# Performance work log

Measured on AMD Instinct MI355X. Metric: run time of the kernel, lower is better.

Reference implementation:

```python
import jax, jax.numpy as jnp
import numpy as np

C1, C2 = 128, 128

def _glorot(key, shape):
    fan_in = shape[-1]
    return jax.random.normal(key, shape, dtype=jnp.float32) / np.sqrt(fan_in)

def setup_inputs() -> dict:
    key = jax.random.key(0)
    ks = jax.random.split(key, 12)
    b, n = 16, 64
    x = jax.random.normal(ks[0], (b, n, 16), dtype=jnp.float32)
    # 1x1 Conv1d weights stored as [out, in]
    e1_w = _glorot(ks[1], (128, 3));    e1_b = jnp.zeros((128,), jnp.float32)
    e2_w = _glorot(ks[2], (128, 13));   e2_b = jnp.zeros((128,), jnp.float32)
    r1_w = _glorot(ks[3], (256, 128));  r1_b = jnp.zeros((256,), jnp.float32)
    r2_w = _glorot(ks[4], (512, 256));  r2_b = jnp.zeros((512,), jnp.float32)
    r3_w = _glorot(ks[5], (1024, 512)); r3_b = jnp.zeros((1024,), jnp.float32)
    w1   = _glorot(ks[6], (512, 2048)); b1   = jnp.zeros((512,), jnp.float32)
    w2   = _glorot(ks[7], (2048, 512)); b2   = jnp.zeros((2048,), jnp.float32)
    return {"x": x, "e1_w": e1_w, "e1_b": e1_b, "e2_w": e2_w, "e2_b": e2_b,
            "r1_w": r1_w, "r1_b": r1_b, "r2_w": r2_w, "r2_b": r2_b,
            "r3_w": r3_w, "r3_b": r3_b, "w1": w1, "b1": b1, "w2": w2, "b2": b2}

def reference(x, e1_w, e1_b, e2_w, e2_b, r1_w, r1_b, r2_w, r2_b, r3_w, r3_b, w1, b1, w2, b2):
    # x: [b, n, 16]; coord = first 3 dims, pos = last 13 (one-hot-like keypoint id)
    coord, pos = x[:, :, :3], x[:, :, 3:]
    # 1x1 Conv1d == per-point linear. E1/E2 each have their own ReLU, then sum.
    emb = (jax.nn.relu(jnp.einsum('bnc,oc->bno', coord, e1_w) + e1_b)
           + jax.nn.relu(jnp.einsum('bnc,oc->bno', pos, e2_w) + e2_b))  # [b,n,128]
    # refine_E: three 1x1 conv + relu stages -> [b,n,1024]
    emb = jax.nn.relu(jnp.einsum('bnc,oc->bno', emb, r1_w) + r1_b)
    emb = jax.nn.relu(jnp.einsum('bnc,oc->bno', emb, r2_w) + r2_b)
    emb = jax.nn.relu(jnp.einsum('bnc,oc->bno', emb, r3_w) + r3_b)
    # Pairwise layer1: cat((emb_i, emb_j), ch) with emb_i[b,c,i,j]=emb[b,c,j],
    # emb_j[b,c,i,j]=emb[b,c,i]. A 1x1 conv on the concat decomposes into
    # two matmuls applied to emb, broadcast-added pairwise (never forming the
    # [b,2048,n,n] tensor).
    w1a, w1b = w1[:, :1024], w1[:, 1024:]
    A = jnp.einsum('bnc,oc->bno', emb, w1a)  # depends on j
    B = jnp.einsum('bnc,oc->bno', emb, w1b)  # depends on i
    h1 = jax.nn.relu(B[:, :, None, :] + A[:, None, :, :] + b1)  # [b,i,j,512]
    # reduction='mean' over (i,j); layer2 (1x1 conv, linear) commutes with mean
    m = jnp.mean(h1, axis=(1, 2))                 # [b,512]
    out = jnp.einsum('bc,oc->bo', m, w2) + b2     # [b,2048]
    return out
```

## Files before the change

### kernel.cpp

```cpp
#include <hip/hip_runtime.h>


typedef __attribute__((ext_vector_type(8))) short s16x8;
typedef __attribute__((ext_vector_type(8))) unsigned short u16x8;
typedef __attribute__((ext_vector_type(4))) float f32x4;

static __device__ __forceinline__ unsigned short f2bf(float f) {
    unsigned u = __float_as_uint(f);
    u += 0x7fff + ((u >> 16) & 1);
    return (unsigned short)(u >> 16);
}

__global__ __launch_bounds__(256) void k_embed(
    const float* __restrict__ x,
    const float* __restrict__ e1w, const float* __restrict__ e1b,
    const float* __restrict__ e2w, const float* __restrict__ e2b,
    unsigned short* __restrict__ emb0b)
{
    int idx = blockIdx.x * 256 + threadIdx.x;
    int row = idx >> 7, o = idx & 127;
    const float* xr = x + row * 16;
    float s1 = e1b[o] + xr[0] * e1w[o * 3 + 0] + xr[1] * e1w[o * 3 + 1] + xr[2] * e1w[o * 3 + 2];
    float s2 = e2b[o];
#pragma unroll
    for (int k = 0; k < 13; ++k) s2 += xr[3 + k] * e2w[o * 13 + k];
    emb0b[row * 128 + o] = f2bf(fmaxf(s1, 0.f) + fmaxf(s2, 0.f));
}

__global__ __launch_bounds__(256) void k_convw(
    const float* __restrict__ r1w, const float* __restrict__ r2w,
    const float* __restrict__ r3w, const float* __restrict__ w1,
    unsigned short* __restrict__ r1b, unsigned short* __restrict__ r2b,
    unsigned short* __restrict__ r3b, unsigned short* __restrict__ wab)
{
    const int n1 = 256 * 128, n2 = 512 * 256, n3 = 1024 * 512;
    int i = (blockIdx.x * 256 + threadIdx.x) * 4;
    float4 v; unsigned short* dst; int j;
    if (i < n1)                { j = i;             v = *(const float4*)(r1w + j); dst = r1b + j; }
    else if (i < n1 + n2)      { j = i - n1;        v = *(const float4*)(r2w + j); dst = r2b + j; }
    else if (i < n1 + n2 + n3) { j = i - n1 - n2;   v = *(const float4*)(r3w + j); dst = r3b + j; }
    else {
        j = i - n1 - n2 - n3;
        int n = j >> 10, k = j & 1023;
        v = *(const float4*)(w1 + (size_t)(n & 511) * 2048 + (n >> 9) * 1024 + k);
        dst = wab + j;
    }
    ushort4 o; o.x = f2bf(v.x); o.y = f2bf(v.y); o.z = f2bf(v.z); o.w = f2bf(v.w);
    *(ushort4*)dst = o;
}

__global__ __launch_bounds__(256) void k_mgemm(
    const unsigned short* __restrict__ A, const unsigned short* __restrict__ W,
    const float* __restrict__ bias, float* __restrict__ Cf,
    unsigned short* __restrict__ Cb, int K, int N, int relu)
{
    __shared__ unsigned short As[64 * 72];
    __shared__ unsigned short Ws[64 * 72];
    int t = threadIdx.x;
    int m0 = blockIdx.x * 64, n0 = blockIdx.y * 64;
    int lane = t & 63, wv = t >> 6;
    int wm = (wv >> 1) * 32, wn = (wv & 1) * 32;
    int lr = lane & 15, quad = lane >> 4;

    f32x4 acc[2][2] = {};

    int srow = t >> 3;
    int scol = (t & 7) * 8;

    for (int k0 = 0; k0 < K; k0 += 64) {
        u16x8 a0 = *(const u16x8*)(A + (size_t)(m0 + srow) * K + k0 + scol);
        u16x8 a1 = *(const u16x8*)(A + (size_t)(m0 + srow + 32) * K + k0 + scol);
        u16x8 w0 = *(const u16x8*)(W + (size_t)(n0 + srow) * K + k0 + scol);
        u16x8 w1 = *(const u16x8*)(W + (size_t)(n0 + srow + 32) * K + k0 + scol);
        __syncthreads();
        *(u16x8*)(As + srow * 72 + scol)        = a0;
        *(u16x8*)(As + (srow + 32) * 72 + scol) = a1;
        *(u16x8*)(Ws + srow * 72 + scol)        = w0;
        *(u16x8*)(Ws + (srow + 32) * 72 + scol) = w1;
        __syncthreads();
#pragma unroll
        for (int kk = 0; kk < 64; kk += 32) {
            s16x8 af[2], bfr[2];
#pragma unroll
            for (int mt = 0; mt < 2; ++mt)
                af[mt] = *(const s16x8*)(As + (wm + mt * 16 + lr) * 72 + kk + quad * 8);
#pragma unroll
            for (int nt = 0; nt < 2; ++nt)
                bfr[nt] = *(const s16x8*)(Ws + (wn + nt * 16 + lr) * 72 + kk + quad * 8);
#pragma unroll
            for (int mt = 0; mt < 2; ++mt)
#pragma unroll
                for (int nt = 0; nt < 2; ++nt)
                    acc[mt][nt] = __builtin_amdgcn_mfma_f32_16x16x32_bf16(
                        af[mt], bfr[nt], acc[mt][nt], 0, 0, 0);
        }
    }

#pragma unroll
    for (int mt = 0; mt < 2; ++mt)
#pragma unroll
        for (int nt = 0; nt < 2; ++nt) {
            int col = n0 + wn + nt * 16 + lr;
            float bv = bias ? bias[col] : 0.f;
#pragma unroll
            for (int r = 0; r < 4; ++r) {
                int row = m0 + wm + mt * 16 + quad * 4 + r;
                float v = acc[mt][nt][r] + bv;
                if (relu) v = fmaxf(v, 0.f);
                if (Cb) Cb[(size_t)row * N + col] = f2bf(v);
                else    Cf[(size_t)row * N + col] = v;
            }
        }
}

__global__ __launch_bounds__(256) void k_pairmean(
    const float* __restrict__ AB, const float* __restrict__ b1,
    float* __restrict__ msum)
{
    __shared__ float sA[64 * 64];
    __shared__ float sB[16 * 64];
    __shared__ float sb1[64];
    __shared__ float sPart[4][64];
    int t = threadIdx.x;
    int b = blockIdx.x, c0 = blockIdx.y * 64, z = blockIdx.z;
    int cl = t & 63, ig = t >> 6;

#pragma unroll
    for (int rep = 0; rep < 4; ++rep) {
        int lin = rep * 256 + t;
        int j = lin >> 4, cq = (lin & 15) * 4;
        float4 v = *(const float4*)(AB + (size_t)(b * 64 + j) * 1024 + c0 + cq);
        *(float4*)&sA[j * 64 + cq] = v;
    }
    {
        int i = t >> 4, cq = (t & 15) * 4;
        float4 v = *(const float4*)(AB + (size_t)(b * 64 + z * 16 + i) * 1024 + 512 + c0 + cq);
        *(float4*)&sB[i * 64 + cq] = v;
    }
    if (t < 64) sb1[t] = b1[c0 + t];
    __syncthreads();

    float av[64];
#pragma unroll
    for (int j = 0; j < 64; ++j) av[j] = sA[j * 64 + cl];
    float b1c = sb1[cl];
    float s = 0.f;
#pragma unroll
    for (int ii = 0; ii < 4; ++ii) {
        float base = sB[(ig * 4 + ii) * 64 + cl] + b1c;
#pragma unroll
        for (int j = 0; j < 64; ++j) s += fmaxf(base + av[j], 0.f);
    }
    sPart[ig][cl] = s;
    __syncthreads();
    if (t < 64) {
        float tot = sPart[0][t] + sPart[1][t] + sPart[2][t] + sPart[3][t];
        atomicAdd(&msum[b * 512 + c0 + t], tot);
    }
}

__global__ __launch_bounds__(256) void k_final(
    const float* __restrict__ msum, const float* __restrict__ w2,
    const float* __restrict__ b2, float* __restrict__ out)
{
    __shared__ float sm[512];
    int t = threadIdx.x;
    int b = blockIdx.x;
    int o = blockIdx.y * 256 + t;
    sm[t]       = msum[b * 512 + t]       * (1.f / 4096.f);
    sm[t + 256] = msum[b * 512 + 256 + t] * (1.f / 4096.f);
    __syncthreads();
    const float* wr = w2 + (size_t)o * 512;
    float acc = 0.f;
#pragma unroll 8
    for (int c = 0; c < 512; c += 4) {
        float4 w = *(const float4*)(wr + c);
        acc += sm[c] * w.x + sm[c + 1] * w.y + sm[c + 2] * w.z + sm[c + 3] * w.w;
    }
    out[b * 2048 + o] = acc + b2[o];
}

extern "C" void kernel_launch(void* const* d_in, const int* in_sizes, int n_in,
                              void* d_out, int out_size, void* d_ws, size_t ws_size,
                              hipStream_t stream)
{
    const float* x   = (const float*)d_in[0];
    const float* e1w = (const float*)d_in[1];
    const float* e1b = (const float*)d_in[2];
    const float* e2w = (const float*)d_in[3];
    const float* e2b = (const float*)d_in[4];
    const float* r1w = (const float*)d_in[5];
    const float* r1b = (const float*)d_in[6];
    const float* r2w = (const float*)d_in[7];
    const float* r2b = (const float*)d_in[8];
    const float* r3w = (const float*)d_in[9];
    const float* r3b = (const float*)d_in[10];
    const float* w1  = (const float*)d_in[11];
    const float* b1  = (const float*)d_in[12];
    const float* w2  = (const float*)d_in[13];
    const float* b2  = (const float*)d_in[14];
    float* out = (float*)d_out;

    unsigned short* emb0b = (unsigned short*)d_ws;
    unsigned short* emb1b = emb0b + 1024 * 128;
    unsigned short* emb2b = emb1b + 1024 * 256;
    unsigned short* emb3b = emb2b + 1024 * 512;
    unsigned short* r1wb  = emb3b + 1024 * 1024;
    unsigned short* r2wb  = r1wb  + 256 * 128;
    unsigned short* r3wb  = r2wb  + 512 * 256;
    unsigned short* wab   = r3wb  + 1024 * 512;
    float* AB   = (float*)(wab + 1024 * 1024);
    float* msum = AB + 1024 * 1024;

    hipMemsetAsync(msum, 0, 16 * 512 * sizeof(float), stream);

    k_convw<<<1696, 256, 0, stream>>>(r1w, r2w, r3w, w1, r1wb, r2wb, r3wb, wab);
    k_embed<<<512, 256, 0, stream>>>(x, e1w, e1b, e2w, e2b, emb0b);

    k_mgemm<<<dim3(16, 4),  256, 0, stream>>>(emb0b, r1wb, r1b, nullptr, emb1b, 128, 256, 1);
    k_mgemm<<<dim3(16, 8),  256, 0, stream>>>(emb1b, r2wb, r2b, nullptr, emb2b, 256, 512, 1);
    k_mgemm<<<dim3(16, 16), 256, 0, stream>>>(emb2b, r3wb, r3b, nullptr, emb3b, 512, 1024, 1);
    k_mgemm<<<dim3(16, 16), 256, 0, stream>>>(emb3b, wab, nullptr, AB, nullptr, 1024, 1024, 0);

    k_pairmean<<<dim3(16, 8, 4), 256, 0, stream>>>(AB, b1, msum);
    k_final<<<dim3(16, 8), 256, 0, stream>>>(msum, w2, b2, out);
}
```

Baseline: 140.6 us.

## Merge setup kernels with memset, halve GEMM M-tile, prefetch next K-slice

The weight-conversion kernel, the embedding kernel and the msum memset become one launch, split by block-index range. The GEMM M tile drops from 64 to 32 rows, doubling the grid for better CU occupancy on these small GEMMs. Global loads for the next K slice are register-prefetched to overlap with MFMA work. Each block now reuses the W tile across fewer rows, so total W traffic rises.

After: 132.7 us. -5.7%, faster.

```diff
diff --git a/kernel.cpp b/kernel.cpp
--- a/kernel.cpp
+++ b/kernel.cpp
@@ -11,42 +11,47 @@
     return (unsigned short)(u >> 16);
 }
 
-__global__ __launch_bounds__(256) void k_embed(
+__global__ __launch_bounds__(256) void k_setup(
     const float* __restrict__ x,
     const float* __restrict__ e1w, const float* __restrict__ e1b,
     const float* __restrict__ e2w, const float* __restrict__ e2b,
-    unsigned short* __restrict__ emb0b)
-{
-    int idx = blockIdx.x * 256 + threadIdx.x;
-    int row = idx >> 7, o = idx & 127;
-    const float* xr = x + row * 16;
-    float s1 = e1b[o] + xr[0] * e1w[o * 3 + 0] + xr[1] * e1w[o * 3 + 1] + xr[2] * e1w[o * 3 + 2];
-    float s2 = e2b[o];
-#pragma unroll
-    for (int k = 0; k < 13; ++k) s2 += xr[3 + k] * e2w[o * 13 + k];
-    emb0b[row * 128 + o] = f2bf(fmaxf(s1, 0.f) + fmaxf(s2, 0.f));
-}
-
-__global__ __launch_bounds__(256) void k_convw(
     const float* __restrict__ r1w, const float* __restrict__ r2w,
     const float* __restrict__ r3w, const float* __restrict__ w1,
-    unsigned short* __restrict__ r1b, unsigned short* __restrict__ r2b,
-    unsigned short* __restrict__ r3b, unsigned short* __restrict__ wab)
-{
-    const int n1 = 256 * 128, n2 = 512 * 256, n3 = 1024 * 512;
-    int i = (blockIdx.x * 256 + threadIdx.x) * 4;
-    float4 v; unsigned short* dst; int j;
-    if (i < n1)                { j = i;             v = *(const float4*)(r1w + j); dst = r1b + j; }
-    else if (i < n1 + n2)      { j = i - n1;        v = *(const float4*)(r2w + j); dst = r2b + j; }
-    else if (i < n1 + n2 + n3) { j = i - n1 - n2;   v = *(const float4*)(r3w + j); dst = r3b + j; }
-    else {
-        j = i - n1 - n2 - n3;
-        int n = j >> 10, k = j & 1023;
-        v = *(const float4*)(w1 + (size_t)(n & 511) * 2048 + (n >> 9) * 1024 + k);
-        dst = wab + j;
-    }
-    ushort4 o; o.x = f2bf(v.x); o.y = f2bf(v.y); o.z = f2bf(v.z); o.w = f2bf(v.w);
-    *(ushort4*)dst = o;
+    unsigned short* __restrict__ emb0b,
+    unsigned short* __restrict__ r1wb, unsigned short* __restrict__ r2wb,
+    unsigned short* __restrict__ r3wb, unsigned short* __restrict__ wab,
+    float* __restrict__ msum)
+{
+    int blk = blockIdx.x;
+    if (blk < 1696) {
+        const int n1 = 256 * 128, n2 = 512 * 256, n3 = 1024 * 512;
+        int i = (blk * 256 + threadIdx.x) * 4;
+        float4 v; unsigned short* dst; int j;
+        if (i < n1)                { j = i;           v = *(const float4*)(r1w + j); dst = r1wb + j; }
+        else if (i < n1 + n2)      { j = i - n1;      v = *(const float4*)(r2w + j); dst = r2wb + j; }
+        else if (i < n1 + n2 + n3) { j = i - n1 - n2; v = *(const float4*)(r3w + j); dst = r3wb + j; }
+        else {
+            j = i - n1 - n2 - n3;
+            int n = j >> 10, k = j & 1023;
+            v = *(const float4*)(w1 + (size_t)(n & 511) * 2048 + (n >> 9) * 1024 + k);
+            dst = wab + j;
+        }
+        ushort4 o; o.x = f2bf(v.x); o.y = f2bf(v.y); o.z = f2bf(v.z); o.w = f2bf(v.w);
+        *(ushort4*)dst = o;
+    } else if (blk < 2208) {
+        int idx = (blk - 1696) * 256 + threadIdx.x;
+        int row = idx >> 7, o = idx & 127;
+        const float* xr = x + row * 16;
+        float s1 = e1b[o] + xr[0] * e1w[o * 3 + 0] + xr[1] * e1w[o * 3 + 1] + xr[2] * e1w[o * 3 + 2];
+        float s2 = e2b[o];
+#pragma unroll
+        for (int k = 0; k < 13; ++k) s2 += xr[3 + k] * e2w[o * 13 + k];
+        emb0b[row * 128 + o] = f2bf(fmaxf(s1, 0.f) + fmaxf(s2, 0.f));
+    } else {
+        int i = ((blk - 2208) * 256 + threadIdx.x) * 4;
+        float4 z = {0.f, 0.f, 0.f, 0.f};
+        *(float4*)(msum + i) = z;
+    }
 }
 
 __global__ __launch_bounds__(256) void k_mgemm(
@@ -54,63 +59,60 @@
     const float* __restrict__ bias, float* __restrict__ Cf,
     unsigned short* __restrict__ Cb, int K, int N, int relu)
 {
-    __shared__ unsigned short As[64 * 72];
+    __shared__ unsigned short As[32 * 72];
     __shared__ unsigned short Ws[64 * 72];
     int t = threadIdx.x;
-    int m0 = blockIdx.x * 64, n0 = blockIdx.y * 64;
+    int m0 = blockIdx.x * 32, n0 = blockIdx.y * 64;
     int lane = t & 63, wv = t >> 6;
-    int wm = (wv >> 1) * 32, wn = (wv & 1) * 32;
+    int wm = (wv >> 1) * 16, wn = (wv & 1) * 32;
     int lr = lane & 15, quad = lane >> 4;
 
-    f32x4 acc[2][2] = {};
+    f32x4 acc[2] = {};
 
     int srow = t >> 3;
     int scol = (t & 7) * 8;
+    const unsigned short* Ap  = A + (size_t)(m0 + srow) * K + scol;
+    const unsigned short* Wp0 = W + (size_t)(n0 + srow) * K + scol;
+    const unsigned short* Wp1 = W + (size_t)(n0 + srow + 32) * K + scol;
+
+    u16x8 ra = *(const u16x8*)Ap;
+    u16x8 rw0 = *(const u16x8*)Wp0;
+    u16x8 rw1 = *(const u16x8*)Wp1;
 
     for (int k0 = 0; k0 < K; k0 += 64) {
-        u16x8 a0 = *(const u16x8*)(A + (size_t)(m0 + srow) * K + k0 + scol);
-        u16x8 a1 = *(const u16x8*)(A + (size_t)(m0 + srow + 32) * K + k0 + scol);
-        u16x8 w0 = *(const u16x8*)(W + (size_t)(n0 + srow) * K + k0 + scol);
-        u16x8 w1 = *(const u16x8*)(W + (size_t)(n0 + srow + 32) * K + k0 + scol);
         __syncthreads();
-        *(u16x8*)(As + srow * 72 + scol)        = a0;
-        *(u16x8*)(As + (srow + 32) * 72 + scol) = a1;
-        *(u16x8*)(Ws + srow * 72 + scol)        = w0;
-        *(u16x8*)(Ws + (srow + 32) * 72 + scol) = w1;
+        *(u16x8*)(As + srow * 72 + scol)        = ra;
+        *(u16x8*)(Ws + srow * 72 + scol)        = rw0;
+        *(u16x8*)(Ws + (srow + 32) * 72 + scol) = rw1;
         __syncthreads();
+        if (k0 + 64 < K) {
+            ra  = *(const u16x8*)(Ap  + k0 + 64);
+            rw0 = *(const u16x8*)(Wp0 + k0 + 64);
+            rw1 = *(const u16x8*)(Wp1 + k0 + 64);
+        }
 #pragma unroll
         for (int kk = 0; kk < 64; kk += 32) {
-            s16x8 af[2], bfr[2];
-#pragma unroll
-            for (int mt = 0; mt < 2; ++mt)
-                af[mt] = *(const s16x8*)(As + (wm + mt * 16 + lr) * 72 + kk + quad * 8);
-#pragma unroll
-            for (int nt = 0; nt < 2; ++nt)
-                bfr[nt] = *(const s16x8*)(Ws + (wn + nt * 16 + lr) * 72 + kk + quad * 8);
-#pragma unroll
-            for (int mt = 0; mt < 2; ++mt)
-#pragma unroll
-                for (int nt = 0; nt < 2; ++nt)
-                    acc[mt][nt] = __builtin_amdgcn_mfma_f32_16x16x32_bf16(
-                        af[mt], bfr[nt], acc[mt][nt], 0, 0, 0);
-        }
-    }
-
-#pragma unroll
-    for (int mt = 0; mt < 2; ++mt)
-#pragma unroll
-        for (int nt = 0; nt < 2; ++nt) {
-            int col = n0 + wn + nt * 16 + lr;
-            float bv = bias ? bias[col] : 0.f;
-#pragma unroll
-            for (int r = 0; r < 4; ++r) {
-                int row = m0 + wm + mt * 16 + quad * 4 + r;
-                float v = acc[mt][nt][r] + bv;
-                if (relu) v = fmaxf(v, 0.f);
-                if (Cb) Cb[(size_t)row * N + col] = f2bf(v);
-                else    Cf[(size_t)row * N + col] = v;
-            }
-        }
+            s16x8 af  = *(const s16x8*)(As + (wm + lr) * 72 + kk + quad * 8);
+            s16x8 bf0 = *(const s16x8*)(Ws + (wn + lr) * 72 + kk + quad * 8);
+            s16x8 bf1 = *(const s16x8*)(Ws + (wn + 16 + lr) * 72 + kk + quad * 8);
+            acc[0] = __builtin_amdgcn_mfma_f32_16x16x32_bf16(af, bf0, acc[0], 0, 0, 0);
+            acc[1] = __builtin_amdgcn_mfma_f32_16x16x32_bf16(af, bf1, acc[1], 0, 0, 0);
+        }
+    }
+
+#pragma unroll
+    for (int nt = 0; nt < 2; ++nt) {
+        int col = n0 + wn + nt * 16 + lr;
+        float bv = bias ? bias[col] : 0.f;
+#pragma unroll
+        for (int r = 0; r < 4; ++r) {
+            int row = m0 + wm + quad * 4 + r;
+            float v = acc[nt][r] + bv;
+            if (relu) v = fmaxf(v, 0.f);
+            if (Cb) Cb[(size_t)row * N + col] = f2bf(v);
+            else    Cf[(size_t)row * N + col] = v;
+        }
+    }
 }
 
 __global__ __launch_bounds__(256) void k_pairmean(
@@ -212,15 +214,14 @@
     float* AB   = (float*)(wab + 1024 * 1024);
     float* msum = AB + 1024 * 1024;
 
-    hipMemsetAsync(msum, 0, 16 * 512 * sizeof(float), stream);
-
-    k_convw<<<1696, 256, 0, stream>>>(r1w, r2w, r3w, w1, r1wb, r2wb, r3wb, wab);
-    k_embed<<<512, 256, 0, stream>>>(x, e1w, e1b, e2w, e2b, emb0b);
-
-    k_mgemm<<<dim3(16, 4),  256, 0, stream>>>(emb0b, r1wb, r1b, nullptr, emb1b, 128, 256, 1);
-    k_mgemm<<<dim3(16, 8),  256, 0, stream>>>(emb1b, r2wb, r2b, nullptr, emb2b, 256, 512, 1);
-    k_mgemm<<<dim3(16, 16), 256, 0, stream>>>(emb2b, r3wb, r3b, nullptr, emb3b, 512, 1024, 1);
-    k_mgemm<<<dim3(16, 16), 256, 0, stream>>>(emb3b, wab, nullptr, AB, nullptr, 1024, 1024, 0);
+    k_setup<<<2216, 256, 0, stream>>>(x, e1w, e1b, e2w, e2b,
+                                      r1w, r2w, r3w, w1,
+                                      emb0b, r1wb, r2wb, r3wb, wab, msum);
+
+    k_mgemm<<<dim3(32, 4),  256, 0, stream>>>(emb0b, r1wb, r1b, nullptr, emb1b, 128, 256, 1);
+    k_mgemm<<<dim3(32, 8),  256, 0, stream>>>(emb1b, r2wb, r2b, nullptr, emb2b, 256, 512, 1);
+    k_mgemm<<<dim3(32, 16), 256, 0, stream>>>(emb2b, r3wb, r3b, nullptr, emb3b, 512, 1024, 1);
+    k_mgemm<<<dim3(32, 16), 256, 0, stream>>>(emb3b, wab, nullptr, AB, nullptr, 1024, 1024, 0);
 
     k_pairmean<<<dim3(16, 8, 4), 256, 0, stream>>>(AB, b1, msum);
     k_final<<<dim3(16, 8), 256, 0, stream>>>(msum, w2, b2, out);
```

## Fuse whole pipeline into one cooperative persistent kernel with grid syncs

Applied to the files above, without the earlier changes.

Replaces the eight separate launches (weight conversion, embed, four GEMMs, pair-mean, final linear) with a single cooperative kernel of 256 blocks that separates stages with grid.sync. Weight bf16 conversion moves inline into each GEMM's shared-memory staging, so the separate conversion pass and its workspace traffic go away. The embed stage is fused into the first GEMM, and the pair-mean reduction is retiled so each block writes a partial sum directly, removing the atomics and the memset. The cost is grid-wide barrier overhead and idle blocks in the small stages, and the weights are reconverted on every call.

New measurement: 299.6 us. 2.13x slower.

```diff
diff --git a/kernel.cpp b/kernel.cpp
--- a/kernel.cpp
+++ b/kernel.cpp
@@ -1,4 +1,7 @@
 #include <hip/hip_runtime.h>
+#include <hip/hip_cooperative_groups.h>
+
+namespace cg = cooperative_groups;
 
 
 typedef __attribute__((ext_vector_type(8))) short s16x8;
@@ -10,92 +13,72 @@
     u += 0x7fff + ((u >> 16) & 1);
     return (unsigned short)(u >> 16);
 }
-
-__global__ __launch_bounds__(256) void k_embed(
-    const float* __restrict__ x,
-    const float* __restrict__ e1w, const float* __restrict__ e1b,
-    const float* __restrict__ e2w, const float* __restrict__ e2b,
-    unsigned short* __restrict__ emb0b)
+static __device__ __forceinline__ u16x8 cvt8(float4 a, float4 b) {
+    u16x8 r;
+    r[0] = f2bf(a.x); r[1] = f2bf(a.y); r[2] = f2bf(a.z); r[3] = f2bf(a.w);
+    r[4] = f2bf(b.x); r[5] = f2bf(b.y); r[6] = f2bf(b.z); r[7] = f2bf(b.w);
+    return r;
+}
+
+struct P {
+    const float *x, *e1w, *e1b, *e2w, *e2b;
+    const float *r1w, *r1b, *r2w, *r2b, *r3w, *r3b;
+    const float *w1, *b1, *w2, *b2;
+    unsigned short *emb1, *emb2, *emb3;
+    float *AB, *msum, *out;
+};
+
+#define SMEM_BYTES 40960
+
+static __device__ __forceinline__ void gemm_tile(
+    const unsigned short* __restrict__ A, const float* __restrict__ Wf,
+    const float* __restrict__ bias, unsigned short* __restrict__ Cb,
+    float* __restrict__ Cf, int K, int N, int m0, int n0,
+    int g4, int relu, int t, unsigned char* smem)
 {
-    int idx = blockIdx.x * 256 + threadIdx.x;
-    int row = idx >> 7, o = idx & 127;
-    const float* xr = x + row * 16;
-    float s1 = e1b[o] + xr[0] * e1w[o * 3 + 0] + xr[1] * e1w[o * 3 + 1] + xr[2] * e1w[o * 3 + 2];
-    float s2 = e2b[o];
-#pragma unroll
-    for (int k = 0; k < 13; ++k) s2 += xr[3 + k] * e2w[o * 13 + k];
-    emb0b[row * 128 + o] = f2bf(fmaxf(s1, 0.f) + fmaxf(s2, 0.f));
-}
-
-__global__ __launch_bounds__(256) void k_convw(
-    const float* __restrict__ r1w, const float* __restrict__ r2w,
-    const float* __restrict__ r3w, const float* __restrict__ w1,
-    unsigned short* __restrict__ r1b, unsigned short* __restrict__ r2b,
-    unsigned short* __restrict__ r3b, unsigned short* __restrict__ wab)
-{
-    const int n1 = 256 * 128, n2 = 512 * 256, n3 = 1024 * 512;
-    int i = (blockIdx.x * 256 + threadIdx.x) * 4;
-    float4 v; unsigned short* dst; int j;
-    if (i < n1)                { j = i;             v = *(const float4*)(r1w + j); dst = r1b + j; }
-    else if (i < n1 + n2)      { j = i - n1;        v = *(const float4*)(r2w + j); dst = r2b + j; }
-    else if (i < n1 + n2 + n3) { j = i - n1 - n2;   v = *(const float4*)(r3w + j); dst = r3b + j; }
-    else {
-        j = i - n1 - n2 - n3;
-        int n = j >> 10, k = j & 1023;
-        v = *(const float4*)(w1 + (size_t)(n & 511) * 2048 + (n >> 9) * 1024 + k);
-        dst = wab + j;
-    }
-    ushort4 o; o.x = f2bf(v.x); o.y = f2bf(v.y); o.z = f2bf(v.z); o.w = f2bf(v.w);
-    *(ushort4*)dst = o;
-}
-
-__global__ __launch_bounds__(256) void k_mgemm(
-    const unsigned short* __restrict__ A, const unsigned short* __restrict__ W,
-    const float* __restrict__ bias, float* __restrict__ Cf,
-    unsigned short* __restrict__ Cb, int K, int N, int relu)
-{
-    __shared__ unsigned short As[64 * 72];
-    __shared__ unsigned short Ws[64 * 72];
-    int t = threadIdx.x;
-    int m0 = blockIdx.x * 64, n0 = blockIdx.y * 64;
+    unsigned short* As = (unsigned short*)smem;
+    unsigned short* Ws = As + 64 * 72;
     int lane = t & 63, wv = t >> 6;
     int wm = (wv >> 1) * 32, wn = (wv & 1) * 32;
     int lr = lane & 15, quad = lane >> 4;
+    int r = t >> 2, q = t & 3;
+
+    const unsigned short* arow = A + (size_t)(m0 + r) * K + q * 16;
+    int n = n0 + r;
+    const float* wrow = g4 ? Wf + (size_t)(n & 511) * 2048 + (n >> 9) * 1024 + q * 16
+                           : Wf + (size_t)n * K + q * 16;
 
     f32x4 acc[2][2] = {};
-
-    int srow = t >> 3;
-    int scol = (t & 7) * 8;
-
     for (int k0 = 0; k0 < K; k0 += 64) {
-        u16x8 a0 = *(const u16x8*)(A + (size_t)(m0 + srow) * K + k0 + scol);
-        u16x8 a1 = *(const u16x8*)(A + (size_t)(m0 + srow + 32) * K + k0 + scol);
-        u16x8 w0 = *(const u16x8*)(W + (size_t)(n0 + srow) * K + k0 + scol);
-        u16x8 w1 = *(const u16x8*)(W + (size_t)(n0 + srow + 32) * K + k0 + scol);
-        __syncthreads();
-        *(u16x8*)(As + srow * 72 + scol)        = a0;
-        *(u16x8*)(As + (srow + 32) * 72 + scol) = a1;
-        *(u16x8*)(Ws + srow * 72 + scol)        = w0;
-        *(u16x8*)(Ws + (srow + 32) * 72 + scol) = w1;
+        u16x8 a0 = *(const u16x8*)(arow + k0);
+        u16x8 a1 = *(const u16x8*)(arow + k0 + 8);
+        float4 w0 = *(const float4*)(wrow + k0);
+        float4 w1v = *(const float4*)(wrow + k0 + 4);
+        float4 w2v = *(const float4*)(wrow + k0 + 8);
+        float4 w3v = *(const float4*)(wrow + k0 + 12);
+        __syncthreads();
+        *(u16x8*)(As + r * 72 + q * 16)     = a0;
+        *(u16x8*)(As + r * 72 + q * 16 + 8) = a1;
+        *(u16x8*)(Ws + r * 72 + q * 16)     = cvt8(w0, w1v);
+        *(u16x8*)(Ws + r * 72 + q * 16 + 8) = cvt8(w2v, w3v);
         __syncthreads();
 #pragma unroll
         for (int kk = 0; kk < 64; kk += 32) {
-            s16x8 af[2], bfr[2];
+            s16x8 af[2], bf[2];
 #pragma unroll
             for (int mt = 0; mt < 2; ++mt)
                 af[mt] = *(const s16x8*)(As + (wm + mt * 16 + lr) * 72 + kk + quad * 8);
 #pragma unroll
             for (int nt = 0; nt < 2; ++nt)
-                bfr[nt] = *(const s16x8*)(Ws + (wn + nt * 16 + lr) * 72 + kk + quad * 8);
+                bf[nt] = *(const s16x8*)(Ws + (wn + nt * 16 + lr) * 72 + kk + quad * 8);
 #pragma unroll
             for (int mt = 0; mt < 2; ++mt)
 #pragma unroll
                 for (int nt = 0; nt < 2; ++nt)
                     acc[mt][nt] = __builtin_amdgcn_mfma_f32_16x16x32_bf16(
-                        af[mt], bfr[nt], acc[mt][nt], 0, 0, 0);
-        }
-    }
-
+                        af[mt], bf[nt], acc[mt][nt], 0, 0, 0);
+        }
+    }
 #pragma unroll
     for (int mt = 0; mt < 2; ++mt)
 #pragma unroll
@@ -103,9 +86,9 @@
             int col = n0 + wn + nt * 16 + lr;
             float bv = bias ? bias[col] : 0.f;
 #pragma unroll
-            for (int r = 0; r < 4; ++r) {
-                int row = m0 + wm + mt * 16 + quad * 4 + r;
-                float v = acc[mt][nt][r] + bv;
+            for (int rr = 0; rr < 4; ++rr) {
+                int row = m0 + wm + mt * 16 + quad * 4 + rr;
+                float v = acc[mt][nt][rr] + bv;
                 if (relu) v = fmaxf(v, 0.f);
                 if (Cb) Cb[(size_t)row * N + col] = f2bf(v);
                 else    Cf[(size_t)row * N + col] = v;
@@ -113,115 +96,179 @@
         }
 }
 
-__global__ __launch_bounds__(256) void k_pairmean(
-    const float* __restrict__ AB, const float* __restrict__ b1,
-    float* __restrict__ msum)
+__global__ __launch_bounds__(256, 2) void k_fused(P p)
 {
-    __shared__ float sA[64 * 64];
-    __shared__ float sB[16 * 64];
-    __shared__ float sb1[64];
-    __shared__ float sPart[4][64];
-    int t = threadIdx.x;
-    int b = blockIdx.x, c0 = blockIdx.y * 64, z = blockIdx.z;
-    int cl = t & 63, ig = t >> 6;
-
-#pragma unroll
-    for (int rep = 0; rep < 4; ++rep) {
-        int lin = rep * 256 + t;
-        int j = lin >> 4, cq = (lin & 15) * 4;
-        float4 v = *(const float4*)(AB + (size_t)(b * 64 + j) * 1024 + c0 + cq);
-        *(float4*)&sA[j * 64 + cq] = v;
-    }
+    __shared__ __align__(16) unsigned char smem[SMEM_BYTES];
+    cg::grid_group grid = cg::this_grid();
+    int t = threadIdx.x, blk = blockIdx.x;
+
+    if (blk < 64) {
+        int m0 = (blk >> 2) * 64, n0 = (blk & 3) * 64;
+        float* xs   = (float*)smem;
+        float* e1ws = xs + 1024;
+        float* e2ws = e1ws + 384;
+        float* e1bs = e2ws + 1664;
+        float* e2bs = e1bs + 128;
+        unsigned short* emb0 = (unsigned short*)(e2bs + 128);
+        unsigned short* Ws   = emb0 + 64 * 136;
+
+        *(float4*)(xs + t * 4) = *(const float4*)(p.x + (size_t)m0 * 16 + t * 4);
+        if (t < 96) *(float4*)(e1ws + t * 4) = *(const float4*)(p.e1w + t * 4);
+        for (int i = t; i < 416; i += 256)
+            *(float4*)(e2ws + i * 4) = *(const float4*)(p.e2w + i * 4);
+        if (t < 128) { e1bs[t] = p.e1b[t]; e2bs[t] = p.e2b[t]; }
+        __syncthreads();
+        for (int idx = t; idx < 8192; idx += 256) {
+            int rr = idx >> 7, o = idx & 127;
+            const float* xr = xs + rr * 16;
+            float s1 = e1bs[o] + xr[0] * e1ws[o * 3] + xr[1] * e1ws[o * 3 + 1]
+                               + xr[2] * e1ws[o * 3 + 2];
+            float s2 = e2bs[o];
+#pragma unroll
+            for (int k = 0; k < 13; ++k) s2 += xr[3 + k] * e2ws[o * 13 + k];
+            emb0[rr * 136 + o] = f2bf(fmaxf(s1, 0.f) + fmaxf(s2, 0.f));
+        }
+
+        int lane = t & 63, wv = t >> 6;
+        int wm = (wv >> 1) * 32, wn = (wv & 1) * 32;
+        int lr = lane & 15, quad = lane >> 4;
+        int r = t >> 2, q = t & 3;
+        const float* wrow = p.r1w + (size_t)(n0 + r) * 128 + q * 16;
+        f32x4 acc[2][2] = {};
+        for (int k0 = 0; k0 < 128; k0 += 64) {
+            float4 w0 = *(const float4*)(wrow + k0);
+            float4 w1v = *(const float4*)(wrow + k0 + 4);
+            float4 w2v = *(const float4*)(wrow + k0 + 8);
+            float4 w3v = *(const float4*)(wrow + k0 + 12);
+            __syncthreads();
+            *(u16x8*)(Ws + r * 72 + q * 16)     = cvt8(w0, w1v);
+            *(u16x8*)(Ws + r * 72 + q * 16 + 8) = cvt8(w2v, w3v);
+            __syncthreads();
+#pragma unroll
+            for (int kk = 0; kk < 64; kk += 32) {
+                s16x8 af[2], bf[2];
+#pragma unroll
+                for (int mt = 0; mt < 2; ++mt)
+                    af[mt] = *(const s16x8*)(emb0 + (wm + mt * 16 + lr) * 136 + k0 + kk + quad * 8);
+#pragma unroll
+                for (int nt = 0; nt < 2; ++nt)
+                    bf[nt] = *(const s16x8*)(Ws + (wn + nt * 16 + lr) * 72 + kk + quad * 8);
+#pragma unroll
+                for (int mt = 0; mt < 2; ++mt)
+#pragma unroll
+                    for (int nt = 0; nt < 2; ++nt)
+                        acc[mt][nt] = __builtin_amdgcn_mfma_f32_16x16x32_bf16(
+                            af[mt], bf[nt], acc[mt][nt], 0, 0, 0);
+            }
+        }
+#pragma unroll
+        for (int mt = 0; mt < 2; ++mt)
+#pragma unroll
+            for (int nt = 0; nt < 2; ++nt) {
+                int col = n0 + wn + nt * 16 + lr;
+                float bv = p.r1b[col];
+#pragma unroll
+                for (int rr = 0; rr < 4; ++rr) {
+                    int row = m0 + wm + mt * 16 + quad * 4 + rr;
+                    p.emb1[(size_t)row * 256 + col] = f2bf(fmaxf(acc[mt][nt][rr] + bv, 0.f));
+                }
+            }
+    }
+    grid.sync();
+
+    if (blk < 128)
+        gemm_tile(p.emb1, p.r2w, p.r2b, p.emb2, nullptr, 256, 512,
+                  (blk >> 3) * 64, (blk & 7) * 64, 0, 1, t, smem);
+    grid.sync();
+
+    gemm_tile(p.emb2, p.r3w, p.r3b, p.emb3, nullptr, 512, 1024,
+              (blk >> 4) * 64, (blk & 15) * 64, 0, 1, t, smem);
+    grid.sync();
+
+    gemm_tile(p.emb3, p.w1, nullptr, nullptr, p.AB, 1024, 1024,
+              (blk >> 4) * 64, (blk & 15) * 64, 1, 0, t, smem);
+    grid.sync();
+
     {
-        int i = t >> 4, cq = (t & 15) * 4;
-        float4 v = *(const float4*)(AB + (size_t)(b * 64 + z * 16 + i) * 1024 + 512 + c0 + cq);
-        *(float4*)&sB[i * 64 + cq] = v;
-    }
-    if (t < 64) sb1[t] = b1[c0 + t];
-    __syncthreads();
-
-    float av[64];
-#pragma unroll
-    for (int j = 0; j < 64; ++j) av[j] = sA[j * 64 + cl];
-    float b1c = sb1[cl];
-    float s = 0.f;
-#pragma unroll
-    for (int ii = 0; ii < 4; ++ii) {
-        float base = sB[(ig * 4 + ii) * 64 + cl] + b1c;
-#pragma unroll
-        for (int j = 0; j < 64; ++j) s += fmaxf(base + av[j], 0.f);
-    }
-    sPart[ig][cl] = s;
-    __syncthreads();
-    if (t < 64) {
-        float tot = sPart[0][t] + sPart[1][t] + sPart[2][t] + sPart[3][t];
-        atomicAdd(&msum[b * 512 + c0 + t], tot);
-    }
-}
-
-__global__ __launch_bounds__(256) void k_final(
-    const float* __restrict__ msum, const float* __restrict__ w2,
-    const float* __restrict__ b2, float* __restrict__ out)
-{
-    __shared__ float sm[512];
-    int t = threadIdx.x;
-    int b = blockIdx.x;
-    int o = blockIdx.y * 256 + t;
-    sm[t]       = msum[b * 512 + t]       * (1.f / 4096.f);
-    sm[t + 256] = msum[b * 512 + 256 + t] * (1.f / 4096.f);
-    __syncthreads();
-    const float* wr = w2 + (size_t)o * 512;
-    float acc = 0.f;
+        int ub = blk >> 4, cc = (blk & 15) * 32;
+        float* pA    = (float*)smem;
+        float* pB    = pA + 2048;
+        float* sb1   = pB + 2048;
+        float* sPart = sb1 + 32;
+        int row = t >> 2, coff = (t & 3) * 8;
+        const float* src = p.AB + (size_t)(ub * 64 + row) * 1024 + cc + coff;
+        *(float4*)(pA + row * 32 + coff)     = *(const float4*)(src);
+        *(float4*)(pA + row * 32 + coff + 4) = *(const float4*)(src + 4);
+        *(float4*)(pB + row * 32 + coff)     = *(const float4*)(src + 512);
+        *(float4*)(pB + row * 32 + coff + 4) = *(const float4*)(src + 516);
+        if (t < 32) sb1[t] = p.b1[cc + t];
+        __syncthreads();
+        int c = t & 31, ii = t >> 5;
+        float bv[8];
+#pragma unroll
+        for (int i = 0; i < 8; ++i) bv[i] = pB[(ii * 8 + i) * 32 + c] + sb1[c];
+        float s = 0.f;
+        for (int j = 0; j < 64; ++j) {
+            float a = pA[j * 32 + c];
+#pragma unroll
+            for (int i = 0; i < 8; ++i) s += fmaxf(bv[i] + a, 0.f);
+        }
+        sPart[ii * 32 + c] = s;
+        __syncthreads();
+        if (t < 32) {
+            float tot = 0.f;
+#pragma unroll
+            for (int i = 0; i < 8; ++i) tot += sPart[i * 32 + t];
+            p.msum[ub * 512 + cc + t] = tot;
+        }
+    }
+    grid.sync();
+
+    {
+        float* sm = (float*)smem;
+        for (int u = blk; u < 512; u += 256) {
+            int b = u >> 5, oc = (u & 31) * 64;
+            __syncthreads();
+            if (t < 128) *(float4*)(sm + t * 4) = *(const float4*)(p.msum + b * 512 + t * 4);
+            __syncthreads();
+            int o = oc + (t >> 2), kq = (t & 3) * 128;
+            const float* wr = p.w2 + (size_t)o * 512 + kq;
+            float acc = 0.f;
 #pragma unroll 8
-    for (int c = 0; c < 512; c += 4) {
-        float4 w = *(const float4*)(wr + c);
-        acc += sm[c] * w.x + sm[c + 1] * w.y + sm[c + 2] * w.z + sm[c + 3] * w.w;
-    }
-    out[b * 2048 + o] = acc + b2[o];
+            for (int k = 0; k < 128; k += 4) {
+                float4 w = *(const float4*)(wr + k);
+                acc += sm[kq + k] * w.x + sm[kq + k + 1] * w.y
+                     + sm[kq + k + 2] * w.z + sm[kq + k + 3] * w.w;
+            }
+            acc += __shfl_xor(acc, 1);
+            acc += __shfl_xor(acc, 2);
+            if ((t & 3) == 0) p.out[b * 2048 + o] = acc * (1.f / 4096.f) + p.b2[o];
+        }
+    }
 }
 
 extern "C" void kernel_launch(void* const* d_in, const int* in_sizes, int n_in,
                               void* d_out, int out_size, void* d_ws, size_t ws_size,
                               hipStream_t stream)
 {
-    const float* x   = (const float*)d_in[0];
-    const float* e1w = (const float*)d_in[1];
-    const float* e1b = (const float*)d_in[2];
-    const float* e2w = (const float*)d_in[3];
-    const float* e2b = (const float*)d_in[4];
-    const float* r1w = (const float*)d_in[5];
-    const float* r1b = (const float*)d_in[6];
-    const float* r2w = (const float*)d_in[7];
-    const float* r2b = (const float*)d_in[8];
-    const float* r3w = (const float*)d_in[9];
-    const float* r3b = (const float*)d_in[10];
-    const float* w1  = (const float*)d_in[11];
-    const float* b1  = (const float*)d_in[12];
-    const float* w2  = (const float*)d_in[13];
-    const float* b2  = (const float*)d_in[14];
-    float* out = (float*)d_out;
-
-    unsigned short* emb0b = (unsigned short*)d_ws;
-    unsigned short* emb1b = emb0b + 1024 * 128;
-    unsigned short* emb2b = emb1b + 1024 * 256;
-    unsigned short* emb3b = emb2b + 1024 * 512;
-    unsigned short* r1wb  = emb3b + 1024 * 1024;
-    unsigned short* r2wb  = r1wb  + 256 * 128;
-    unsigned short* r3wb  = r2wb  + 512 * 256;
-    unsigned short* wab   = r3wb  + 1024 * 512;
-    float* AB   = (float*)(wab + 1024 * 1024);
-    float* msum = AB + 1024 * 1024;
-
-    hipMemsetAsync(msum, 0, 16 * 512 * sizeof(float), stream);
-
-    k_convw<<<1696, 256, 0, stream>>>(r1w, r2w, r3w, w1, r1wb, r2wb, r3wb, wab);
-    k_embed<<<512, 256, 0, stream>>>(x, e1w, e1b, e2w, e2b, emb0b);
-
-    k_mgemm<<<dim3(16, 4),  256, 0, stream>>>(emb0b, r1wb, r1b, nullptr, emb1b, 128, 256, 1);
-    k_mgemm<<<dim3(16, 8),  256, 0, stream>>>(emb1b, r2wb, r2b, nullptr, emb2b, 256, 512, 1);
-    k_mgemm<<<dim3(16, 16), 256, 0, stream>>>(emb2b, r3wb, r3b, nullptr, emb3b, 512, 1024, 1);
-    k_mgemm<<<dim3(16, 16), 256, 0, stream>>>(emb3b, wab, nullptr, AB, nullptr, 1024, 1024, 0);
-
-    k_pairmean<<<dim3(16, 8, 4), 256, 0, stream>>>(AB, b1, msum);
-    k_final<<<dim3(16, 8), 256, 0, stream>>>(msum, w2, b2, out);
-}
+    P p;
+    p.x   = (const float*)d_in[0];
+    p.e1w = (const float*)d_in[1];  p.e1b = (const float*)d_in[2];
+    p.e2w = (const float*)d_in[3];  p.e2b = (const float*)d_in[4];
+    p.r1w = (const float*)d_in[5];  p.r1b = (const float*)d_in[6];
+    p.r2w = (const float*)d_in[7];  p.r2b = (const float*)d_in[8];
+    p.r3w = (const float*)d_in[9];  p.r3b = (const float*)d_in[10];
+    p.w1  = (const float*)d_in[11]; p.b1  = (const float*)d_in[12];
+    p.w2  = (const float*)d_in[13]; p.b2  = (const float*)d_in[14];
+    p.out = (float*)d_out;
+
+    unsigned short* w = (unsigned short*)d_ws;
+    p.emb1 = w;
+    p.emb2 = p.emb1 + 1024 * 256;
+    p.emb3 = p.emb2 + 1024 * 512;
+    p.AB   = (float*)(p.emb3 + 1024 * 1024);
+    p.msum = p.AB + 1024 * 1024;
+
+    void* args[] = { &p };
+    hipLaunchCooperativeKernel((void*)k_fused, dim3(256), dim3(256), args, 0, stream);
+}
```
